# Performance work log

Measured on AMD Instinct MI355X. Metric: run time of the kernel, lower is better.

Reference implementation:

```python
import jax, jax.numpy as jnp
import numpy as np

COMMITMENT_COST = 0.25


def setup_inputs() -> dict:
    key = jax.random.key(0)
    k1, k2 = jax.random.split(key)
    x = jax.random.normal(k1, (32, 256, 32, 32), dtype=jnp.float32)
    codebook = jax.random.normal(k2, (1024, 256), dtype=jnp.float32) * 0.02
    return {"x": x, "codebook": codebook}


def reference(x, codebook):
    # x: [B, C, H, W] -> z: [B, H, W, C] (NHWC), C = embedding_dim
    B, C, H, W = x.shape
    z = jnp.transpose(x, (0, 2, 3, 1))
    zf = z.reshape(-1, C)  # [N, C], N = B*H*W
    # squared euclidean distance: ||z||^2 - 2 z.e + ||e||^2  -> [N, K]
    d = (
        jnp.sum(zf * zf, axis=-1, keepdims=True)
        - 2.0 * (zf @ codebook.T)
        + jnp.sum(codebook * codebook, axis=-1)
    )
    encoding_indices = jnp.argmin(d, axis=1)  # [N]
    quantized = codebook[encoding_indices].reshape(z.shape)  # [B, H, W, C]

    # training losses (entropy_loss_ratio == 0 -> entropy branch skipped)
    sg = jax.lax.stop_gradient
    e_latent_loss = jnp.mean((sg(quantized) - z) ** 2) * COMMITMENT_COST
    q_latent_loss = jnp.mean((quantized - sg(z)) ** 2)
    quantizer_loss = e_latent_loss + q_latent_loss

    # straight-through estimator
    quantized_st = z + sg(quantized - z)
    out = jnp.transpose(quantized_st, (0, 3, 1, 2))  # back to NCHW
    return out, quantizer_loss, e_latent_loss, q_latent_loss, encoding_indices
```

## Files before the change

kernel.cpp:

```cpp
#include <hip/hip_runtime.h>
#include <cfloat>

#define C_DIM   256
#define HW      1024
#define N_ROWS  32768
#define K_CODES 1024
#define ROWS    32
#define NCHUNK  16
#define WCHUNK_BYTES 8192
#define LISTCAP 128
#define DELTA   0.008f
#define CMASK   0xFFFFFFF0u

#define OUT_ELEMS 8388608
#define LOSS_OFF  8388608
#define IDX_OFF   8388611

typedef _Float16 half8 __attribute__((ext_vector_type(8)));
typedef _Float16 f16x4 __attribute__((ext_vector_type(4)));
typedef float    f32x4 __attribute__((ext_vector_type(4)));

#define AS1 __attribute__((address_space(1)))
#define AS3 __attribute__((address_space(3)))

#define OFF_EBUF  0
#define OFF_EN    32768
#define OFF_S32   36864
#define OFF_M1W   36992
#define OFF_THR   37504
#define OFF_RES   37632
#define OFF_FIDX  37888
#define OFF_LCNT  38016
#define OFF_LMETA 38144
#define SMEM_BYTES 40192

#define QT_STRIDE 258

#define DPP_MIN(x, ctrl) fminf((x), __int_as_float(__builtin_amdgcn_update_dpp(0, __float_as_int(x), (ctrl), 0xf, 0xf, true)))

__global__ void prep_kernel(const float* __restrict__ cb, float* __restrict__ enorm,
                            char* __restrict__ cb16) {
    int k = blockIdx.x * 4 + (threadIdx.x >> 6);
    int lane = threadIdx.x & 63;
    int c0 = lane * 4;
    float4 v = *(const float4*)(cb + k * C_DIM + c0);
    double s = (double)v.x * v.x + (double)v.y * v.y + (double)v.z * v.z + (double)v.w * v.w;
    #pragma unroll
    for (int m = 1; m < 64; m <<= 1) s += __shfl_xor(s, m, 64);
    if (lane == 0) enorm[k] = (float)s;
    f16x4 h;
    h[0] = (_Float16)v.x; h[1] = (_Float16)v.y; h[2] = (_Float16)v.z; h[3] = (_Float16)v.w;
    int dst = ((k >> 4) << 13) + ((c0 >> 5) << 10) + (((c0 >> 3) & 3) << 8)
            + ((k & 15) << 4) + ((c0 & 7) << 1);
    *(f16x4*)(cb16 + dst) = h;
}

__global__ __launch_bounds__(256, 2) void vq_main(
    const float* __restrict__ x, const float* __restrict__ cb,
    const float* __restrict__ enorm_g, const char* __restrict__ cb16,
    float* __restrict__ out, float* __restrict__ idx_out, float* __restrict__ t2_out)
{
    extern __shared__ char smem[];
    float* qt      = (float*)(smem + OFF_EBUF);
    float* en_lds  = (float*)(smem + OFF_EN);
    float* S32     = (float*)(smem + OFF_S32);
    float* m1w     = (float*)(smem + OFF_M1W);
    float* thr     = (float*)(smem + OFF_THR);
    unsigned long long* res = (unsigned long long*)(smem + OFF_RES);
    int*   fidx    = (int*)(smem + OFF_FIDX);
    int*   lcnt    = (int*)(smem + OFF_LCNT);
    unsigned int* lmeta = (unsigned int*)(smem + OFF_LMETA);

    const int t    = threadIdx.x;
    const int lane = t & 63;
    const int wq   = t >> 6;
    const int l15  = lane & 15;
    const int l4   = lane >> 4;
    const int row0 = blockIdx.x * ROWS;
    const int b    = row0 >> 10;
    const int hw0  = row0 & 1023;
    const float* xb = x + b * (C_DIM * HW) + hw0;

    char* ebw = smem + OFF_EBUF + wq * WCHUNK_BYTES;
    const char* cbw = cb16 + wq * (NCHUNK * WCHUNK_BYTES);

    #pragma unroll
    for (int i = 0; i < 8; i++) {
        __builtin_amdgcn_global_load_lds((const AS1 unsigned int*)(cbw + i * 1024 + lane * 16),
                                         (AS3 unsigned int*)(ebw + i * 1024), 16, 0, 0);
    }

    *(float4*)&en_lds[t * 4] = *(const float4*)(enorm_g + t * 4);
    if (t < 4) lcnt[t] = 0;

    half8 af[2][8];
    double s64[2] = {0.0, 0.0};
    #pragma unroll
    for (int rt = 0; rt < 2; rt++) {
        const float* xr = xb + rt * 16 + l15;
        #pragma unroll
        for (int kk = 0; kk < 8; kk++) {
            float v[8];
            #pragma unroll
            for (int j = 0; j < 8; j++) v[j] = xr[(kk * 32 + l4 * 8 + j) * HW];
            #pragma unroll
            for (int j = 0; j < 8; j++) s64[rt] = fma((double)v[j], (double)v[j], s64[rt]);
            half8 h;
            #pragma unroll
            for (int j = 0; j < 8; j++) h[j] = (_Float16)(-2.0f * v[j]);
            af[rt][kk] = h;
        }
    }
    #pragma unroll
    for (int rt = 0; rt < 2; rt++) {
        s64[rt] += __shfl_xor(s64[rt], 16, 64);
        s64[rt] += __shfl_xor(s64[rt], 32, 64);
    }
    if (wq == 0 && l4 == 0) {
        S32[l15]      = (float)s64[0];
        S32[16 + l15] = (float)s64[1];
    }
    __syncthreads();

    const int bbase  = (l4 << 8) + (l15 << 4);
    const int enbase = wq * 256 + l15;

    float u1[2][4], u2[2][4];
    #pragma unroll
    for (int rt = 0; rt < 2; rt++)
        #pragma unroll
        for (int r2 = 0; r2 < 4; r2++) { u1[rt][r2] = FLT_MAX; u2[rt][r2] = FLT_MAX; }

    for (int ch = 0; ch < NCHUNK; ch++) {
        if (ch) { asm volatile("s_waitcnt vmcnt(0)" ::: "memory"); }
        __builtin_amdgcn_sched_barrier(0);

        half8 bf[8];
        #pragma unroll
        for (int kk = 0; kk < 8; kk++)
            bf[kk] = *(const half8*)(ebw + bbase + (kk << 10));
        asm volatile("s_waitcnt lgkmcnt(0)" ::: "memory");
        __builtin_amdgcn_sched_barrier(0);

        if (ch + 1 < NCHUNK) {
            const char* src = cbw + (ch + 1) * WCHUNK_BYTES;
            #pragma unroll
            for (int i = 0; i < 8; i++) {
                __builtin_amdgcn_global_load_lds((const AS1 unsigned int*)(src + i * 1024 + lane * 16),
                                                 (AS3 unsigned int*)(ebw + i * 1024), 16, 0, 0);
            }
        }

        const float en = en_lds[enbase + ch * 16];
        f32x4 acc0 = {en, en, en, en};
        f32x4 acc1 = {en, en, en, en};
        #pragma unroll
        for (int kk = 0; kk < 8; kk++) {
            acc0 = __builtin_amdgcn_mfma_f32_16x16x32_f16(af[0][kk], bf[kk], acc0, 0, 0, 0);
            acc1 = __builtin_amdgcn_mfma_f32_16x16x32_f16(af[1][kk], bf[kk], acc1, 0, 0, 0);
        }
        #pragma unroll
        for (int r2 = 0; r2 < 4; r2++) {
            float ua = __uint_as_float((__float_as_uint(acc0[r2]) & CMASK) | (unsigned)ch);
            u2[0][r2] = __builtin_amdgcn_fmed3f(ua, u1[0][r2], u2[0][r2]);
            u1[0][r2] = fminf(u1[0][r2], ua);
            float ub = __uint_as_float((__float_as_uint(acc1[r2]) & CMASK) | (unsigned)ch);
            u2[1][r2] = __builtin_amdgcn_fmed3f(ub, u1[1][r2], u2[1][r2]);
            u1[1][r2] = fminf(u1[1][r2], ub);
        }
    }

    #pragma unroll
    for (int rt = 0; rt < 2; rt++) {
        #pragma unroll
        for (int r2 = 0; r2 < 4; r2++) {
            float m = u1[rt][r2];
            m = DPP_MIN(m, 0xB1);
            m = DPP_MIN(m, 0x4E);
            m = DPP_MIN(m, 0x141);
            m = DPP_MIN(m, 0x140);
            if (l15 == 0) m1w[wq * 32 + rt * 16 + l4 * 4 + r2] = m;
        }
    }
    __syncthreads();
    if (t < 32) {
        thr[t] = fminf(fminf(m1w[t], m1w[32 + t]), fminf(m1w[64 + t], m1w[96 + t])) + DELTA;
        res[t] = ~0ull;
    }
    __syncthreads();

    #pragma unroll
    for (int rt = 0; rt < 2; rt++) {
        #pragma unroll
        for (int r2 = 0; r2 < 4; r2++) {
            int row_l = rt * 16 + l4 * 4 + r2;
            float tr = thr[row_l];
            if (u1[rt][r2] < tr) {
                int ch1 = (int)(__float_as_uint(u1[rt][r2]) & 15u);
                int code = wq * 256 + ch1 * 16 + l15;
                int slot = atomicAdd(&lcnt[wq], 1);
                if (slot < LISTCAP)
                    lmeta[wq * LISTCAP + slot] = ((unsigned)row_l << 16) | (unsigned)code;
            }
            if (u2[rt][r2] < tr) {
                int ch2 = (int)(__float_as_uint(u2[rt][r2]) & 15u);
                int code = wq * 256 + ch2 * 16 + l15;
                int slot = atomicAdd(&lcnt[wq], 1);
                if (slot < LISTCAP)
                    lmeta[wq * LISTCAP + slot] = ((unsigned)row_l << 16) | (unsigned)code;
            }
        }
    }
    __syncthreads();

    {
        int n = lcnt[wq]; if (n > LISTCAP) n = LISTCAP;
        for (int base = 0; base < n; base += 4) {
            int it = base + l4;
            if (it < n) {
                unsigned meta = lmeta[wq * LISTCAP + it];
                int row  = (int)(meta >> 16);
                int code = (int)(meta & 1023u);
                const float* xr = xb + row;
                const float* er = cb + code * C_DIM;
                double acc = 0.0;
                #pragma unroll
                for (int s2 = 0; s2 < 16; s2++) {
                    int c = l15 + 16 * s2;
                    acc = fma((double)xr[(size_t)c * HW], (double)er[c], acc);
                }
                acc += __shfl_xor(acc, 1, 64);
                acc += __shfl_xor(acc, 2, 64);
                acc += __shfl_xor(acc, 4, 64);
                acc += __shfl_xor(acc, 8, 64);
                if (l15 == 0) {
                    float Mf = (float)acc;
                    float t2 = __fadd_rn(__fsub_rn(S32[row], __fmul_rn(2.0f, Mf)), en_lds[code]);
                    unsigned long long pk =
                        ((unsigned long long)__float_as_uint(t2) << 32) | (unsigned long long)(unsigned)code;
                    atomicMin(&res[row], pk);
                }
            }
        }
    }
    __syncthreads();

    if (t < 32) {
        unsigned long long v = res[t];
        int code = (int)(v & 1023u);
        fidx[t] = code;
        idx_out[row0 + t] = (float)code;
        t2_out[row0 + t] = __uint_as_float((unsigned)(v >> 32));
    }
    __syncthreads();

    {
        for (int idx = t; idx < 32 * 64; idx += 256) {
            int r  = idx >> 6;
            int c4 = idx & 63;
            const float* er = cb + fidx[r] * C_DIM;
            *(float4*)&qt[r * QT_STRIDE + c4 * 4] = *(const float4*)(er + c4 * 4);
        }
        __syncthreads();
        float* ob = out + b * (C_DIM * HW) + hw0;
        int rr = t & 31;
        int cg = t >> 5;
        for (int cc = cg; cc < C_DIM; cc += 8) {
            ob[cc * HW + rr] = qt[rr * QT_STRIDE + cc];
        }
    }
}

__global__ void loss_kernel(const float* __restrict__ t2min, float* __restrict__ losses) {
    __shared__ double sh[256];
    int t = threadIdx.x;
    double a = 0.0;
    const int per = N_ROWS / 256;
    for (int i = t * per; i < t * per + per; i++) a += (double)t2min[i];
    sh[t] = a;
    __syncthreads();
    for (int s = 128; s > 0; s >>= 1) {
        if (t < s) sh[t] += sh[t + s];
        __syncthreads();
    }
    if (t == 0) {
        double M = sh[0] / (double)OUT_ELEMS;
        losses[0] = (float)(1.25 * M);
        losses[1] = (float)(0.25 * M);
        losses[2] = (float)(M);
    }
}

extern "C" void kernel_launch(void* const* d_in, const int* in_sizes, int n_in,
                              void* d_out, int out_size, void* d_ws, size_t ws_size,
                              hipStream_t stream) {
    const float* x  = (const float*)d_in[0];
    const float* cb = (const float*)d_in[1];
    float* out     = (float*)d_out;
    float* losses  = out + LOSS_OFF;
    float* idx_out = out + IDX_OFF;

    char*  cb16     = (char*)d_ws;
    float* t2ws     = (float*)((char*)d_ws + 524288);
    float* enorm_ws = (float*)((char*)d_ws + 524288 + 131072);

    hipFuncSetAttribute(reinterpret_cast<const void*>(vq_main),
                        hipFuncAttributeMaxDynamicSharedMemorySize, SMEM_BYTES);

    prep_kernel<<<K_CODES / 4, 256, 0, stream>>>(cb, enorm_ws, cb16);
    vq_main<<<N_ROWS / ROWS, 256, SMEM_BYTES, stream>>>(x, cb, enorm_ws, cb16, out, idx_out, t2ws);
    loss_kernel<<<1, 256, 0, stream>>>(t2ws, losses);
}
```

Baseline: 77.14 us.

## Double rows per block and double-buffer codebook chunks in LDS

```diff
diff --git a/kernel.cpp b/kernel.cpp
--- a/kernel.cpp
+++ b/kernel.cpp
@@ -5,7 +5,7 @@
 #define HW      1024
 #define N_ROWS  32768
 #define K_CODES 1024
-#define ROWS    32
+#define ROWS    64
 #define NCHUNK  16
 #define WCHUNK_BYTES 8192
 #define LISTCAP 128
@@ -24,15 +24,15 @@
 #define AS3 __attribute__((address_space(3)))
 
 #define OFF_EBUF  0
-#define OFF_EN    32768
-#define OFF_S32   36864
-#define OFF_M1W   36992
-#define OFF_THR   37504
-#define OFF_RES   37632
-#define OFF_FIDX  37888
-#define OFF_LCNT  38016
-#define OFF_LMETA 38144
-#define SMEM_BYTES 40192
+#define OFF_EN    65536
+#define OFF_S32   69632
+#define OFF_M1W   69888
+#define OFF_THR   70912
+#define OFF_RES   71168
+#define OFF_FIDX  71680
+#define OFF_LCNT  71936
+#define OFF_LMETA 72192
+#define SMEM_BYTES 74240
 
 #define QT_STRIDE 258
 
@@ -81,22 +81,27 @@
     const int hw0  = row0 & 1023;
     const float* xb = x + b * (C_DIM * HW) + hw0;
 
-    char* ebw = smem + OFF_EBUF + wq * WCHUNK_BYTES;
+    char* ebw = smem + OFF_EBUF + wq * (2 * WCHUNK_BYTES);
     const char* cbw = cb16 + wq * (NCHUNK * WCHUNK_BYTES);
 
     #pragma unroll
-    for (int i = 0; i < 8; i++) {
-        __builtin_amdgcn_global_load_lds((const AS1 unsigned int*)(cbw + i * 1024 + lane * 16),
-                                         (AS3 unsigned int*)(ebw + i * 1024), 16, 0, 0);
+    for (int c2 = 0; c2 < 2; c2++) {
+        const char* src = cbw + c2 * WCHUNK_BYTES;
+        char* dst = ebw + c2 * WCHUNK_BYTES;
+        #pragma unroll
+        for (int i = 0; i < 8; i++) {
+            __builtin_amdgcn_global_load_lds((const AS1 unsigned int*)(src + i * 1024 + lane * 16),
+                                             (AS3 unsigned int*)(dst + i * 1024), 16, 0, 0);
+        }
     }
 
     *(float4*)&en_lds[t * 4] = *(const float4*)(enorm_g + t * 4);
     if (t < 4) lcnt[t] = 0;
 
-    half8 af[2][8];
-    double s64[2] = {0.0, 0.0};
-    #pragma unroll
-    for (int rt = 0; rt < 2; rt++) {
+    half8 af[4][8];
+    double s64[4] = {0.0, 0.0, 0.0, 0.0};
+    #pragma unroll
+    for (int rt = 0; rt < 4; rt++) {
         const float* xr = xb + rt * 16 + l15;
         #pragma unroll
         for (int kk = 0; kk < 8; kk++) {
@@ -112,66 +117,79 @@
         }
     }
     #pragma unroll
-    for (int rt = 0; rt < 2; rt++) {
+    for (int rt = 0; rt < 4; rt++) {
         s64[rt] += __shfl_xor(s64[rt], 16, 64);
         s64[rt] += __shfl_xor(s64[rt], 32, 64);
     }
     if (wq == 0 && l4 == 0) {
-        S32[l15]      = (float)s64[0];
-        S32[16 + l15] = (float)s64[1];
+        #pragma unroll
+        for (int rt = 0; rt < 4; rt++) S32[rt * 16 + l15] = (float)s64[rt];
     }
     __syncthreads();
 
     const int bbase  = (l4 << 8) + (l15 << 4);
     const int enbase = wq * 256 + l15;
 
-    float u1[2][4], u2[2][4];
-    #pragma unroll
-    for (int rt = 0; rt < 2; rt++)
+    float u1[4][4], u2[4][4];
+    #pragma unroll
+    for (int rt = 0; rt < 4; rt++)
         #pragma unroll
         for (int r2 = 0; r2 < 4; r2++) { u1[rt][r2] = FLT_MAX; u2[rt][r2] = FLT_MAX; }
 
     for (int ch = 0; ch < NCHUNK; ch++) {
-        if (ch) { asm volatile("s_waitcnt vmcnt(0)" ::: "memory"); }
+        if (ch == NCHUNK - 1) { asm volatile("s_waitcnt vmcnt(0)" ::: "memory"); }
+        else                  { asm volatile("s_waitcnt vmcnt(8)" ::: "memory"); }
         __builtin_amdgcn_sched_barrier(0);
 
+        const char* ebc = ebw + (ch & 1) * WCHUNK_BYTES;
         half8 bf[8];
         #pragma unroll
         for (int kk = 0; kk < 8; kk++)
-            bf[kk] = *(const half8*)(ebw + bbase + (kk << 10));
+            bf[kk] = *(const half8*)(ebc + bbase + (kk << 10));
         asm volatile("s_waitcnt lgkmcnt(0)" ::: "memory");
         __builtin_amdgcn_sched_barrier(0);
 
-        if (ch + 1 < NCHUNK) {
-            const char* src = cbw + (ch + 1) * WCHUNK_BYTES;
+        if (ch + 2 < NCHUNK) {
+            const char* src = cbw + (ch + 2) * WCHUNK_BYTES;
+            char* dst = ebw + (ch & 1) * WCHUNK_BYTES;
             #pragma unroll
             for (int i = 0; i < 8; i++) {
                 __builtin_amdgcn_global_load_lds((const AS1 unsigned int*)(src + i * 1024 + lane * 16),
-                                                 (AS3 unsigned int*)(ebw + i * 1024), 16, 0, 0);
+                                                 (AS3 unsigned int*)(dst + i * 1024), 16, 0, 0);
             }
         }
 
         const float en = en_lds[enbase + ch * 16];
         f32x4 acc0 = {en, en, en, en};
         f32x4 acc1 = {en, en, en, en};
+        f32x4 acc2 = {en, en, en, en};
+        f32x4 acc3 = {en, en, en, en};
         #pragma unroll
         for (int kk = 0; kk < 8; kk++) {
             acc0 = __builtin_amdgcn_mfma_f32_16x16x32_f16(af[0][kk], bf[kk], acc0, 0, 0, 0);
             acc1 = __builtin_amdgcn_mfma_f32_16x16x32_f16(af[1][kk], bf[kk], acc1, 0, 0, 0);
+            acc2 = __builtin_amdgcn_mfma_f32_16x16x32_f16(af[2][kk], bf[kk], acc2, 0, 0, 0);
+            acc3 = __builtin_amdgcn_mfma_f32_16x16x32_f16(af[3][kk], bf[kk], acc3, 0, 0, 0);
         }
         #pragma unroll
         for (int r2 = 0; r2 < 4; r2++) {
-            float ua = __uint_as_float((__float_as_uint(acc0[r2]) & CMASK) | (unsigned)ch);
-            u2[0][r2] = __builtin_amdgcn_fmed3f(ua, u1[0][r2], u2[0][r2]);
-            u1[0][r2] = fminf(u1[0][r2], ua);
-            float ub = __uint_as_float((__float_as_uint(acc1[r2]) & CMASK) | (unsigned)ch);
-            u2[1][r2] = __builtin_amdgcn_fmed3f(ub, u1[1][r2], u2[1][r2]);
-            u1[1][r2] = fminf(u1[1][r2], ub);
-        }
-    }
-
-    #pragma unroll
-    for (int rt = 0; rt < 2; rt++) {
+            float a0 = __uint_as_float((__float_as_uint(acc0[r2]) & CMASK) | (unsigned)ch);
+            u2[0][r2] = __builtin_amdgcn_fmed3f(a0, u1[0][r2], u2[0][r2]);
+            u1[0][r2] = fminf(u1[0][r2], a0);
+            float a1 = __uint_as_float((__float_as_uint(acc1[r2]) & CMASK) | (unsigned)ch);
+            u2[1][r2] = __builtin_amdgcn_fmed3f(a1, u1[1][r2], u2[1][r2]);
+            u1[1][r2] = fminf(u1[1][r2], a1);
+            float a2 = __uint_as_float((__float_as_uint(acc2[r2]) & CMASK) | (unsigned)ch);
+            u2[2][r2] = __builtin_amdgcn_fmed3f(a2, u1[2][r2], u2[2][r2]);
+            u1[2][r2] = fminf(u1[2][r2], a2);
+            float a3 = __uint_as_float((__float_as_uint(acc3[r2]) & CMASK) | (unsigned)ch);
+            u2[3][r2] = __builtin_amdgcn_fmed3f(a3, u1[3][r2], u2[3][r2]);
+            u1[3][r2] = fminf(u1[3][r2], a3);
+        }
+    }
+
+    #pragma unroll
+    for (int rt = 0; rt < 4; rt++) {
         #pragma unroll
         for (int r2 = 0; r2 < 4; r2++) {
             float m = u1[rt][r2];
@@ -179,18 +197,18 @@
             m = DPP_MIN(m, 0x4E);
             m = DPP_MIN(m, 0x141);
             m = DPP_MIN(m, 0x140);
-            if (l15 == 0) m1w[wq * 32 + rt * 16 + l4 * 4 + r2] = m;
-        }
-    }
-    __syncthreads();
-    if (t < 32) {
-        thr[t] = fminf(fminf(m1w[t], m1w[32 + t]), fminf(m1w[64 + t], m1w[96 + t])) + DELTA;
+            if (l15 == 0) m1w[wq * 64 + rt * 16 + l4 * 4 + r2] = m;
+        }
+    }
+    __syncthreads();
+    if (t < 64) {
+        thr[t] = fminf(fminf(m1w[t], m1w[64 + t]), fminf(m1w[128 + t], m1w[192 + t])) + DELTA;
         res[t] = ~0ull;
     }
     __syncthreads();
 
     #pragma unroll
-    for (int rt = 0; rt < 2; rt++) {
+    for (int rt = 0; rt < 4; rt++) {
         #pragma unroll
         for (int r2 = 0; r2 < 4; r2++) {
             int row_l = rt * 16 + l4 * 4 + r2;
@@ -245,28 +263,29 @@
     }
     __syncthreads();
 
-    if (t < 32) {
+    if (t < 64) {
         unsigned long long v = res[t];
         int code = (int)(v & 1023u);
         fidx[t] = code;
         idx_out[row0 + t] = (float)code;
         t2_out[row0 + t] = __uint_as_float((unsigned)(v >> 32));
     }
-    __syncthreads();
-
-    {
+
+    float* ob = out + b * (C_DIM * HW) + hw0;
+    #pragma unroll
+    for (int half = 0; half < 2; half++) {
+        __syncthreads();
         for (int idx = t; idx < 32 * 64; idx += 256) {
             int r  = idx >> 6;
             int c4 = idx & 63;
-            const float* er = cb + fidx[r] * C_DIM;
+            const float* er = cb + fidx[half * 32 + r] * C_DIM;
             *(float4*)&qt[r * QT_STRIDE + c4 * 4] = *(const float4*)(er + c4 * 4);
         }
         __syncthreads();
-        float* ob = out + b * (C_DIM * HW) + hw0;
         int rr = t & 31;
         int cg = t >> 5;
         for (int cc = cg; cc < C_DIM; cc += 8) {
-            ob[cc * HW + rr] = qt[rr * QT_STRIDE + cc];
+            ob[cc * HW + half * 32 + rr] = qt[rr * QT_STRIDE + cc];
         }
     }
 }
```

Result: slower. 93.62 us (+21.4%).
